# Performance work log

Measured on AMD Instinct MI355X. Metric: run time of the kernel, lower is better.

The kernel has to match this reference:

```python
import jax, jax.numpy as jnp
import numpy as np

NUM_NODES = 100000
NUM_EDGES = 1600000
IN_DIM = 128
HID = 128
OUT_DIM = 5


def setup_inputs() -> dict:
    key = jax.random.key(0)
    ks = jax.random.split(key, 8)
    x = jax.random.normal(ks[0], (NUM_NODES, IN_DIM), dtype=jnp.float32)
    edges = jax.random.randint(ks[1], (2, NUM_EDGES), 0, NUM_NODES, dtype=jnp.int32)
    s = 1.0 / np.sqrt(IN_DIM)
    W1 = jax.random.uniform(ks[2], (IN_DIM, HID), jnp.float32, -s, s)
    b1 = jax.random.uniform(ks[3], (HID,), jnp.float32, -s, s)
    sh = 1.0 / np.sqrt(HID)
    W2 = jax.random.uniform(ks[4], (HID, HID), jnp.float32, -sh, sh)
    b2 = jax.random.uniform(ks[5], (HID,), jnp.float32, -sh, sh)
    Wp = jax.random.uniform(ks[6], (HID, OUT_DIM), jnp.float32, -sh, sh)
    bp = jax.random.uniform(ks[7], (OUT_DIM,), jnp.float32, -sh, sh)
    return {"x": x, "edges": edges, "W1": W1, "b1": b1, "W2": W2, "b2": b2, "Wp": Wp, "bp": bp}


def _gnn_layer(x, src, tgt, W, b):
    # scatter-add of source features into targets (mean aggregation)
    agg = jax.ops.segment_sum(x[src], tgt, num_segments=NUM_NODES)  # [N, d]
    cnt = jax.ops.segment_sum(jnp.ones_like(tgt, dtype=x.dtype), tgt, num_segments=NUM_NODES)
    cnt = jnp.maximum(cnt, 1.0)  # clamp(min=1)
    agg = agg / cnt[:, None]
    combined = x + agg  # residual
    return jax.nn.relu(combined @ W + b)


def reference(x, edges, W1, b1, W2, b2, Wp, bp):
    src, tgt = edges[0], edges[1]
    h = _gnn_layer(x, src, tgt, W1, b1)
    h = _gnn_layer(h, src, tgt, W2, b2)
    return h @ Wp + bp  # [N, OUT_DIM]
```

## Files before the change

### kernel.cpp

```cpp
#include <hip/hip_runtime.h>

typedef unsigned int uint32;
typedef unsigned short ushort16;

typedef __attribute__((ext_vector_type(8))) short short8;
typedef __attribute__((ext_vector_type(4))) float f32x4;


#define RSH 11
#define NRG 2048
#define CAP 49152
#define CH  8192

__device__ __forceinline__ ushort16 f2bf(float f) {
    uint32 u = __float_as_uint(f);
    u += 0x7fffu + ((u >> 16) & 1u);
    return (ushort16)(u >> 16);
}
__device__ __forceinline__ float bfhi(uint32 u) { return __uint_as_float(u & 0xffff0000u); }
__device__ __forceinline__ float bflo(uint32 u) { return __uint_as_float(u << 16); }
__device__ __forceinline__ uint32 pack2(float a, float b) {
    return (uint32)f2bf(a) | ((uint32)f2bf(b) << 16);
}

union U16 { uint4 u; short8 s; };
__device__ __forceinline__ short8 ld_frag(const ushort16* p) {
    U16 x; x.u = *(const uint4*)p; return x.s;
}

#define ACC8(v) \
    acc[0] += bflo(v.x); acc[1] += bfhi(v.x); \
    acc[2] += bflo(v.y); acc[3] += bfhi(v.y); \
    acc[4] += bflo(v.z); acc[5] += bfhi(v.z); \
    acc[6] += bflo(v.w); acc[7] += bfhi(v.w);

__global__ __launch_bounds__(256)
void partition_kernel(const int* __restrict__ src, const int* __restrict__ tgt,
                      uint2* __restrict__ rlist, int* __restrict__ rcursor,
                      const float* __restrict__ W1, const float* __restrict__ W2,
                      ushort16* __restrict__ Wt1, ushort16* __restrict__ Wt2,
                      int E, int PB, int R) {
    int tid = threadIdx.x, blk = blockIdx.x;
    if (blk >= PB) {
        const float* W = (blk - PB) ? W2 : W1;
        ushort16* Wt = (blk - PB) ? Wt2 : Wt1;
        for (int i = tid; i < 16384; i += 256) {
            int k = i >> 7, c = i & 127;
            Wt[c * 128 + k] = f2bf(W[i]);
        }
        return;
    }
    __shared__ int cnt[64];
    __shared__ int cbase[64];
    for (int r = tid; r < R; r += 256) cnt[r] = 0;
    __syncthreads();
    int e0 = blk * CH, e1 = min(e0 + CH, E);
    for (int e = e0 + tid; e < e1; e += 256)
        atomicAdd(&cnt[tgt[e] >> RSH], 1);
    __syncthreads();
    for (int r = tid; r < R; r += 256) {
        cbase[r] = atomicAdd(&rcursor[r], cnt[r]);
        cnt[r] = 0;
    }
    __syncthreads();
    for (int e = e0 + tid; e < e1; e += 256) {
        int t = tgt[e];
        int r = t >> RSH;
        int sl = cbase[r] + atomicAdd(&cnt[r], 1);
        if (sl < CAP) rlist[(size_t)r * CAP + sl] = make_uint2((uint32)src[e], (uint32)t);
    }
}

template<int INF32>
__device__ __forceinline__
void gemm_body(const void* __restrict__ Asrc, const ushort16* __restrict__ Wt,
               int M, ushort16* __restrict__ outB, int bid) {
    const int tid = threadIdx.x;
    const int lane = tid & 63;
    const int wave = tid >> 6;
    const int l15 = lane & 15;
    const int quad = lane >> 4;
    const int r0 = bid * 64 + wave * 16;

    int arow = r0 + l15;
    if (arow >= M) arow = M - 1;

    short8 afr[4];
    if (INF32) {
        const float* ap = (const float*)Asrc + (size_t)arow * 128 + quad * 8;
#pragma unroll
        for (int kt = 0; kt < 4; ++kt) {
            float4 a0 = *(const float4*)(ap + kt * 32);
            float4 a1 = *(const float4*)(ap + kt * 32 + 4);
            short8 f;
            f[0] = (short)f2bf(a0.x); f[1] = (short)f2bf(a0.y);
            f[2] = (short)f2bf(a0.z); f[3] = (short)f2bf(a0.w);
            f[4] = (short)f2bf(a1.x); f[5] = (short)f2bf(a1.y);
            f[6] = (short)f2bf(a1.z); f[7] = (short)f2bf(a1.w);
            afr[kt] = f;
        }
    } else {
        const ushort16* aptr = (const ushort16*)Asrc + (size_t)arow * 128 + quad * 8;
#pragma unroll
        for (int kt = 0; kt < 4; ++kt) afr[kt] = ld_frag(aptr + kt * 32);
    }

    f32x4 acc[8];
#pragma unroll
    for (int t = 0; t < 8; ++t) acc[t] = (f32x4){0.f, 0.f, 0.f, 0.f};

#pragma unroll
    for (int t = 0; t < 8; ++t) {
        const ushort16* bptr = Wt + (size_t)(16 * t + l15) * 128 + quad * 8;
        short8 b0 = ld_frag(bptr);
        short8 b1 = ld_frag(bptr + 32);
        short8 b2 = ld_frag(bptr + 64);
        short8 b3 = ld_frag(bptr + 96);
        acc[t] = __builtin_amdgcn_mfma_f32_16x16x32_bf16(afr[0], b0, acc[t], 0, 0, 0);
        acc[t] = __builtin_amdgcn_mfma_f32_16x16x32_bf16(afr[1], b1, acc[t], 0, 0, 0);
        acc[t] = __builtin_amdgcn_mfma_f32_16x16x32_bf16(afr[2], b2, acc[t], 0, 0, 0);
        acc[t] = __builtin_amdgcn_mfma_f32_16x16x32_bf16(afr[3], b3, acc[t], 0, 0, 0);
    }

#pragma unroll
    for (int t = 0; t < 8; ++t) {
        float ov[4];
        ov[0] = acc[t].x; ov[1] = acc[t].y; ov[2] = acc[t].z; ov[3] = acc[t].w;
#pragma unroll
        for (int r = 0; r < 4; ++r) {
            float nb = __shfl_xor(ov[r], 1, 64);
            int row = r0 + quad * 4 + r;
            if (((l15 & 1) == 0) && row < M) {
                *(uint32*)(outB + (size_t)row * 128 + 16 * t + l15) = pack2(ov[r], nb);
            }
        }
    }
}

__global__ __launch_bounds__(256)
void csr_gemm1_kernel(const uint2* __restrict__ rlist, const int* __restrict__ rcursor,
                      int* __restrict__ start, int* __restrict__ deg,
                      int* __restrict__ csr, int N, int R,
                      const float* __restrict__ x, const ushort16* __restrict__ Wt1,
                      ushort16* __restrict__ ybuf) {
    int blk = blockIdx.x;
    if (blk >= R) {
        gemm_body<1>(x, Wt1, N, ybuf, blk - R);
        return;
    }
    int tid = threadIdx.x;
    __shared__ int hist[NRG];
    __shared__ int sd[256];
    __shared__ int carrySh;
    __shared__ int rbaseSh, countSh;

    int r = blk;
    if (tid == 0) {
        int rb = 0;
        for (int i = 0; i < r; ++i) rb += rcursor[i];
        rbaseSh = rb;
        countSh = min(rcursor[r], CAP);
    }
    for (int i = tid; i < NRG; i += 256) hist[i] = 0;
    __syncthreads();
    int count = countSh;
    int rbase = rbaseSh;
    const uint2* rl = rlist + (size_t)r * CAP;
    int n0 = r << RSH;

    for (int i = tid; i < count; i += 256)
        atomicAdd(&hist[rl[i].y & (NRG - 1)], 1);
    __syncthreads();

    if (tid == 0) carrySh = rbase;
    __syncthreads();
    for (int c = 0; c < 8; ++c) {
        int idx = c * 256 + tid;
        int v = hist[idx];
        int c0 = carrySh;
        sd[tid] = v;
        __syncthreads();
        for (int o = 1; o < 256; o <<= 1) {
            int t = (tid >= o) ? sd[tid - o] : 0;
            __syncthreads();
            sd[tid] += t;
            __syncthreads();
        }
        int excl = sd[tid] - v + c0;
        int tot = sd[255];
        int node = n0 + idx;
        if (node < N) { start[node] = excl; deg[node] = v; }
        hist[idx] = excl;
        __syncthreads();
        if (tid == 0) carrySh = c0 + tot;
        __syncthreads();
    }

    for (int i = tid; i < count; i += 256) {
        uint2 e = rl[i];
        int p = atomicAdd(&hist[e.y & (NRG - 1)], 1);
        csr[p] = (int)e.x;
    }
}

template<int INF32>
__global__ __launch_bounds__(256)
void gemm_raw_kernel(const void* __restrict__ Asrc, const ushort16* __restrict__ Wt,
                     int M, ushort16* __restrict__ outB) {
    gemm_body<INF32>(Asrc, Wt, M, outB, blockIdx.x);
}

template<int PROJ>
__global__ __launch_bounds__(256, 4)
void agg_fuse_kernel(const ushort16* __restrict__ hb,
                     const int* __restrict__ start, const int* __restrict__ degv,
                     const int* __restrict__ csr,
                     const float* __restrict__ bias,
                     uint32* __restrict__ outb,
                     const float* __restrict__ Wp, const float* __restrict__ bp,
                     float* __restrict__ outP, int N) {
    int wid = (blockIdx.x * 256 + threadIdx.x) >> 6;
    int lane = threadIdx.x & 63;
    if (wid >= N) return;
    int g = lane >> 4, sl = lane & 15;
    int s0 = start[wid];
    int deg = degv[wid];
    int fi = sl * 4 + g;
    uint32 su = ((const uint32*)hb)[(size_t)wid * 64 + fi];

    float acc[8];
#pragma unroll
    for (int j = 0; j < 8; ++j) acc[j] = 0.f;

    int base = 0;
    for (; base + 8 <= deg; base += 8) {
        int i0 = csr[s0 + base + g];
        int i1 = csr[s0 + base + 4 + g];
        uint4 v0 = *(const uint4*)(hb + (size_t)i0 * 128 + sl * 8);
        uint4 v1 = *(const uint4*)(hb + (size_t)i1 * 128 + sl * 8);
        ACC8(v0); ACC8(v1);
    }
    for (; base < deg; base += 4) {
        int e = base + g;
        if (e < deg) {
            int s = csr[s0 + e];
            uint4 v = *(const uint4*)(hb + (size_t)s * 128 + sl * 8);
            ACC8(v);
        }
    }
#pragma unroll
    for (int j = 0; j < 8; ++j) {
        acc[j] += __shfl_xor(acc[j], 16, 64);
        acc[j] += __shfl_xor(acc[j], 32, 64);
    }
    float inv = 1.f / fmaxf((float)deg, 1.f);
    float ax = (g == 0) ? acc[0] : (g == 1) ? acc[2] : (g == 2) ? acc[4] : acc[6];
    float ay = (g == 0) ? acc[1] : (g == 1) ? acc[3] : (g == 2) ? acc[5] : acc[7];

    float ha = fmaxf(bflo(su) + ax * inv + bias[2 * fi],     0.f);
    float hc = fmaxf(bfhi(su) + ay * inv + bias[2 * fi + 1], 0.f);

    if (!PROJ) {
        outb[(size_t)wid * 64 + fi] = pack2(ha, hc);
    } else {
        float p[5];
#pragma unroll
        for (int j = 0; j < 5; ++j)
            p[j] = ha * Wp[(2 * fi) * 5 + j] + hc * Wp[(2 * fi + 1) * 5 + j];
#pragma unroll
        for (int m = 1; m <= 32; m <<= 1)
#pragma unroll
            for (int j = 0; j < 5; ++j) p[j] += __shfl_xor(p[j], m, 64);
        if (lane == 0) {
#pragma unroll
            for (int j = 0; j < 5; ++j) outP[(size_t)wid * 5 + j] = p[j] + bp[j];
        }
    }
}

extern "C" void kernel_launch(void* const* d_in, const int* in_sizes, int n_in,
                              void* d_out, int out_size, void* d_ws, size_t ws_size,
                              hipStream_t stream) {
    const float* x     = (const float*)d_in[0];
    const int*   edges = (const int*)d_in[1];
    const float* W1    = (const float*)d_in[2];
    const float* b1    = (const float*)d_in[3];
    const float* W2    = (const float*)d_in[4];
    const float* b2    = (const float*)d_in[5];
    const float* Wp    = (const float*)d_in[6];
    const float* bp    = (const float*)d_in[7];
    float* out = (float*)d_out;

    int N = in_sizes[0] / 128;
    int E = in_sizes[1] / 2;
    const int* src = edges;
    const int* tgt = edges + E;

    const int R  = (N + NRG - 1) >> RSH;
    const int PB = (E + CH - 1) / CH;

    char* ws = (char*)d_ws;
    size_t off = 0;
    auto alloc = [&](size_t bytes) {
        char* p = ws + off;
        off = (off + bytes + 255) & ~(size_t)255;
        return p;
    };
    int*      deg     = (int*)alloc((size_t)N * 4);
    int*      start   = (int*)alloc((size_t)N * 4);
    int*      csr     = (int*)alloc((size_t)E * 4);
    uint2*    rlist   = (uint2*)alloc((size_t)R * CAP * 8);
    int*      rcursor = (int*)alloc(64 * 4);
    ushort16* ybuf    = (ushort16*)alloc((size_t)N * 128 * 2);
    ushort16* h1      = (ushort16*)alloc((size_t)N * 128 * 2);
    ushort16* Wt1     = (ushort16*)alloc(128 * 128 * 2);
    ushort16* Wt2     = (ushort16*)alloc(128 * 128 * 2);
    (void)ws_size;

    const int gemmBlocks = (N + 63) / 64;
    const int aggBlocks  = (N + 3) / 4;

    hipMemsetAsync(rcursor, 0, 64 * 4, stream);
    partition_kernel<<<PB + 2, 256, 0, stream>>>(src, tgt, rlist, rcursor,
                                                 W1, W2, Wt1, Wt2, E, PB, R);
    csr_gemm1_kernel<<<R + gemmBlocks, 256, 0, stream>>>(rlist, rcursor, start, deg,
                                                         csr, N, R, x, Wt1, ybuf);
    agg_fuse_kernel<0><<<aggBlocks, 256, 0, stream>>>(ybuf, start, deg, csr, b1,
                                                      (uint32*)h1, nullptr, nullptr,
                                                      nullptr, N);
    gemm_raw_kernel<0><<<gemmBlocks, 256, 0, stream>>>(h1, Wt2, N, ybuf);
    agg_fuse_kernel<1><<<aggBlocks, 256, 0, stream>>>(ybuf, start, deg, csr, b2,
                                                      nullptr, Wp, bp, out, N);
}
```

Baseline: 387.3 us.

## Split edge partition into count, scan, scatter passes and widen CSR build blocks

Replaces the single partition kernel, which used global atomic cursors, with three passes: per-chunk bucket counts, a per-bucket scan across chunks, and a deterministic scatter that reads int4-vectorized edges. Chunk size shrinks to raise parallelism, and the weight transpose is spread over 16 blocks. The CSR build kernel now uses 1024-thread blocks with a 4-way unrolled histogram/scatter and a wave-shuffle prefix for the bucket base. This adds two kernel launches and an extra pass over tgt in exchange for more parallel, contention-free partitioning. Vector loads assume E divisible by 4.

Measured after the change: 325.3 us. -16.0%, faster.

```diff
diff --git a/kernel.cpp b/kernel.cpp
--- a/kernel.cpp
+++ b/kernel.cpp
@@ -10,7 +10,7 @@
 #define RSH 11
 #define NRG 2048
 #define CAP 49152
-#define CH  8192
+#define CH  2048
 
 __device__ __forceinline__ ushort16 f2bf(float f) {
     uint32 u = __float_as_uint(f);
@@ -35,54 +35,111 @@
     acc[6] += bflo(v.w); acc[7] += bfhi(v.w);
 
 __global__ __launch_bounds__(256)
-void partition_kernel(const int* __restrict__ src, const int* __restrict__ tgt,
-                      uint2* __restrict__ rlist, int* __restrict__ rcursor,
-                      const float* __restrict__ W1, const float* __restrict__ W2,
-                      ushort16* __restrict__ Wt1, ushort16* __restrict__ Wt2,
-                      int E, int PB, int R) {
+void count_prep_kernel(const int* __restrict__ tgt, int* __restrict__ hist,
+                       const float* __restrict__ W1, const float* __restrict__ W2,
+                       ushort16* __restrict__ Wt1, ushort16* __restrict__ Wt2,
+                       int E, int PB, int R) {
     int tid = threadIdx.x, blk = blockIdx.x;
     if (blk >= PB) {
-        const float* W = (blk - PB) ? W2 : W1;
-        ushort16* Wt = (blk - PB) ? Wt2 : Wt1;
-        for (int i = tid; i < 16384; i += 256) {
-            int k = i >> 7, c = i & 127;
-            Wt[c * 128 + k] = f2bf(W[i]);
-        }
+        int idx = blk - PB;
+        const float* W = (idx >> 3) ? W2 : W1;
+        ushort16* Wt = (idx >> 3) ? Wt2 : Wt1;
+        int i0 = (idx & 7) * 2048 + tid * 8;
+        float4 a = *(const float4*)(W + i0);
+        float4 b = *(const float4*)(W + i0 + 4);
+        int k = i0 >> 7, col = i0 & 127;
+        Wt[(col + 0) * 128 + k] = f2bf(a.x);
+        Wt[(col + 1) * 128 + k] = f2bf(a.y);
+        Wt[(col + 2) * 128 + k] = f2bf(a.z);
+        Wt[(col + 3) * 128 + k] = f2bf(a.w);
+        Wt[(col + 4) * 128 + k] = f2bf(b.x);
+        Wt[(col + 5) * 128 + k] = f2bf(b.y);
+        Wt[(col + 6) * 128 + k] = f2bf(b.z);
+        Wt[(col + 7) * 128 + k] = f2bf(b.w);
         return;
     }
     __shared__ int cnt[64];
-    __shared__ int cbase[64];
-    for (int r = tid; r < R; r += 256) cnt[r] = 0;
-    __syncthreads();
-    int e0 = blk * CH, e1 = min(e0 + CH, E);
-    for (int e = e0 + tid; e < e1; e += 256)
-        atomicAdd(&cnt[tgt[e] >> RSH], 1);
-    __syncthreads();
-    for (int r = tid; r < R; r += 256) {
-        cbase[r] = atomicAdd(&rcursor[r], cnt[r]);
-        cnt[r] = 0;
-    }
-    __syncthreads();
-    for (int e = e0 + tid; e < e1; e += 256) {
-        int t = tgt[e];
-        int r = t >> RSH;
-        int sl = cbase[r] + atomicAdd(&cnt[r], 1);
-        if (sl < CAP) rlist[(size_t)r * CAP + sl] = make_uint2((uint32)src[e], (uint32)t);
+    if (tid < 64) cnt[tid] = 0;
+    __syncthreads();
+    int q0 = blk * (CH / 4), q1 = min(q0 + CH / 4, E / 4);
+    for (int q = q0 + tid; q < q1; q += 256) {
+        int4 t = ((const int4*)tgt)[q];
+        atomicAdd(&cnt[t.x >> RSH], 1);
+        atomicAdd(&cnt[t.y >> RSH], 1);
+        atomicAdd(&cnt[t.z >> RSH], 1);
+        atomicAdd(&cnt[t.w >> RSH], 1);
+    }
+    __syncthreads();
+    if (tid < R) hist[(size_t)blk * 64 + tid] = cnt[tid];
+}
+
+__global__ __launch_bounds__(256)
+void scan_kernel(int* __restrict__ hist, int* __restrict__ total, int PB) {
+    __shared__ int sd[256];
+    __shared__ int carrySh;
+    int r = blockIdx.x, tid = threadIdx.x;
+    if (tid == 0) carrySh = 0;
+    __syncthreads();
+    int chunks = (PB + 255) >> 8;
+    for (int ch = 0; ch < chunks; ++ch) {
+        int g = ch * 256 + tid;
+        int v = (g < PB) ? hist[(size_t)g * 64 + r] : 0;
+        int c0 = carrySh;
+        sd[tid] = v;
+        __syncthreads();
+        for (int o = 1; o < 256; o <<= 1) {
+            int t = (tid >= o) ? sd[tid - o] : 0;
+            __syncthreads();
+            sd[tid] += t;
+            __syncthreads();
+        }
+        if (g < PB) hist[(size_t)g * 64 + r] = sd[tid] - v + c0;
+        int tot = sd[255];
+        __syncthreads();
+        if (tid == 0) carrySh = c0 + tot;
+        __syncthreads();
+    }
+    if (tid == 0) total[r] = carrySh;
+}
+
+__global__ __launch_bounds__(256)
+void scatter_kernel(const int* __restrict__ src, const int* __restrict__ tgt,
+                    const int* __restrict__ hist, uint2* __restrict__ rlist,
+                    int E, int R) {
+    __shared__ int cb[64];
+    __shared__ int cnt[64];
+    int tid = threadIdx.x, blk = blockIdx.x;
+    if (tid < 64) {
+        cnt[tid] = 0;
+        cb[tid] = (tid < R) ? hist[(size_t)blk * 64 + tid] : 0;
+    }
+    __syncthreads();
+    int q0 = blk * (CH / 4), q1 = min(q0 + CH / 4, E / 4);
+    for (int q = q0 + tid; q < q1; q += 256) {
+        int4 t = ((const int4*)tgt)[q];
+        int4 s = ((const int4*)src)[q];
+        int r0 = t.x >> RSH, r1 = t.y >> RSH, r2 = t.z >> RSH, r3 = t.w >> RSH;
+        int l0 = atomicAdd(&cnt[r0], 1);
+        int l1 = atomicAdd(&cnt[r1], 1);
+        int l2 = atomicAdd(&cnt[r2], 1);
+        int l3 = atomicAdd(&cnt[r3], 1);
+        int p0 = cb[r0] + l0, p1 = cb[r1] + l1, p2 = cb[r2] + l2, p3 = cb[r3] + l3;
+        if (p0 < CAP) rlist[(size_t)r0 * CAP + p0] = make_uint2((uint32)s.x, (uint32)t.x);
+        if (p1 < CAP) rlist[(size_t)r1 * CAP + p1] = make_uint2((uint32)s.y, (uint32)t.y);
+        if (p2 < CAP) rlist[(size_t)r2 * CAP + p2] = make_uint2((uint32)s.z, (uint32)t.z);
+        if (p3 < CAP) rlist[(size_t)r3 * CAP + p3] = make_uint2((uint32)s.w, (uint32)t.w);
     }
 }
 
 template<int INF32>
 __device__ __forceinline__
-void gemm_body(const void* __restrict__ Asrc, const ushort16* __restrict__ Wt,
-               int M, ushort16* __restrict__ outB, int bid) {
-    const int tid = threadIdx.x;
-    const int lane = tid & 63;
-    const int wave = tid >> 6;
+void gemm_rows(const void* __restrict__ Asrc, const ushort16* __restrict__ Wt,
+               int M, ushort16* __restrict__ outB, int r0w) {
+    const int lane = threadIdx.x & 63;
     const int l15 = lane & 15;
     const int quad = lane >> 4;
-    const int r0 = bid * 64 + wave * 16;
-
-    int arow = r0 + l15;
+
+    int arow = r0w + l15;
     if (arow >= M) arow = M - 1;
 
     short8 afr[4];
@@ -129,7 +186,7 @@
 #pragma unroll
         for (int r = 0; r < 4; ++r) {
             float nb = __shfl_xor(ov[r], 1, 64);
-            int row = r0 + quad * 4 + r;
+            int row = r0w + quad * 4 + r;
             if (((l15 & 1) == 0) && row < M) {
                 *(uint32*)(outB + (size_t)row * 128 + 16 * t + l15) = pack2(ov[r], nb);
             }
@@ -137,69 +194,95 @@
     }
 }
 
-__global__ __launch_bounds__(256)
-void csr_gemm1_kernel(const uint2* __restrict__ rlist, const int* __restrict__ rcursor,
+__global__ __launch_bounds__(1024)
+void csr_gemm1_kernel(const uint2* __restrict__ rlist, const int* __restrict__ total,
                       int* __restrict__ start, int* __restrict__ deg,
                       int* __restrict__ csr, int N, int R,
                       const float* __restrict__ x, const ushort16* __restrict__ Wt1,
                       ushort16* __restrict__ ybuf) {
     int blk = blockIdx.x;
+    int tid = threadIdx.x;
     if (blk >= R) {
-        gemm_body<1>(x, Wt1, N, ybuf, blk - R);
+        int gid = blk - R;
+        gemm_rows<1>(x, Wt1, N, ybuf, gid * 256 + (tid >> 6) * 16);
         return;
     }
-    int tid = threadIdx.x;
     __shared__ int hist[NRG];
-    __shared__ int sd[256];
+    __shared__ int sd[1024];
     __shared__ int carrySh;
     __shared__ int rbaseSh, countSh;
 
     int r = blk;
-    if (tid == 0) {
-        int rb = 0;
-        for (int i = 0; i < r; ++i) rb += rcursor[i];
-        rbaseSh = rb;
-        countSh = min(rcursor[r], CAP);
-    }
-    for (int i = tid; i < NRG; i += 256) hist[i] = 0;
+    if (tid == 0) countSh = min(total[r], CAP);
+    if (tid < 64) {
+        int v = (tid < R) ? total[tid] : 0;
+        int pm = (tid < r) ? v : 0;
+#pragma unroll
+        for (int o = 1; o < 64; o <<= 1) pm += __shfl_xor(pm, o, 64);
+        if (tid == 0) rbaseSh = pm;
+    }
+    for (int i = tid; i < NRG; i += 1024) hist[i] = 0;
     __syncthreads();
     int count = countSh;
-    int rbase = rbaseSh;
     const uint2* rl = rlist + (size_t)r * CAP;
     int n0 = r << RSH;
 
-    for (int i = tid; i < count; i += 256)
-        atomicAdd(&hist[rl[i].y & (NRG - 1)], 1);
-    __syncthreads();
-
-    if (tid == 0) carrySh = rbase;
-    __syncthreads();
-    for (int c = 0; c < 8; ++c) {
-        int idx = c * 256 + tid;
+    {
+        int i = tid;
+        for (; i + 3072 < count; i += 4096) {
+            uint2 a = rl[i], b = rl[i + 1024], c = rl[i + 2048], d = rl[i + 3072];
+            atomicAdd(&hist[a.y & (NRG - 1)], 1);
+            atomicAdd(&hist[b.y & (NRG - 1)], 1);
+            atomicAdd(&hist[c.y & (NRG - 1)], 1);
+            atomicAdd(&hist[d.y & (NRG - 1)], 1);
+        }
+        for (; i < count; i += 1024)
+            atomicAdd(&hist[rl[i].y & (NRG - 1)], 1);
+    }
+    __syncthreads();
+
+    if (tid == 0) carrySh = rbaseSh;
+    __syncthreads();
+    for (int ch = 0; ch < 2; ++ch) {
+        int idx = ch * 1024 + tid;
         int v = hist[idx];
         int c0 = carrySh;
         sd[tid] = v;
         __syncthreads();
-        for (int o = 1; o < 256; o <<= 1) {
+        for (int o = 1; o < 1024; o <<= 1) {
             int t = (tid >= o) ? sd[tid - o] : 0;
             __syncthreads();
             sd[tid] += t;
             __syncthreads();
         }
         int excl = sd[tid] - v + c0;
-        int tot = sd[255];
+        int tot = sd[1023];
         int node = n0 + idx;
         if (node < N) { start[node] = excl; deg[node] = v; }
+        __syncthreads();
         hist[idx] = excl;
-        __syncthreads();
         if (tid == 0) carrySh = c0 + tot;
         __syncthreads();
     }
 
-    for (int i = tid; i < count; i += 256) {
-        uint2 e = rl[i];
-        int p = atomicAdd(&hist[e.y & (NRG - 1)], 1);
-        csr[p] = (int)e.x;
+    {
+        int i = tid;
+        for (; i + 3072 < count; i += 4096) {
+            uint2 a = rl[i], b = rl[i + 1024], c = rl[i + 2048], d = rl[i + 3072];
+            int pa = atomicAdd(&hist[a.y & (NRG - 1)], 1);
+            int pb = atomicAdd(&hist[b.y & (NRG - 1)], 1);
+            int pc = atomicAdd(&hist[c.y & (NRG - 1)], 1);
+            int pd = atomicAdd(&hist[d.y & (NRG - 1)], 1);
+            csr[pa] = (int)a.x;
+            csr[pb] = (int)b.x;
+            csr[pc] = (int)c.x;
+            csr[pd] = (int)d.x;
+        }
+        for (; i < count; i += 1024) {
+            uint2 e = rl[i];
+            int p = atomicAdd(&hist[e.y & (NRG - 1)], 1);
+            csr[p] = (int)e.x;
+        }
     }
 }
 
@@ -207,7 +290,7 @@
 __global__ __launch_bounds__(256)
 void gemm_raw_kernel(const void* __restrict__ Asrc, const ushort16* __restrict__ Wt,
                      int M, ushort16* __restrict__ outB) {
-    gemm_body<INF32>(Asrc, Wt, M, outB, blockIdx.x);
+    gemm_rows<INF32>(Asrc, Wt, M, outB, blockIdx.x * 64 + (threadIdx.x >> 6) * 16);
 }
 
 template<int PROJ>
@@ -310,21 +393,24 @@
     int*      start   = (int*)alloc((size_t)N * 4);
     int*      csr     = (int*)alloc((size_t)E * 4);
     uint2*    rlist   = (uint2*)alloc((size_t)R * CAP * 8);
-    int*      rcursor = (int*)alloc(64 * 4);
+    int*      hist    = (int*)alloc((size_t)PB * 64 * 4);
+    int*      total   = (int*)alloc(64 * 4);
     ushort16* ybuf    = (ushort16*)alloc((size_t)N * 128 * 2);
     ushort16* h1      = (ushort16*)alloc((size_t)N * 128 * 2);
     ushort16* Wt1     = (ushort16*)alloc(128 * 128 * 2);
     ushort16* Wt2     = (ushort16*)alloc(128 * 128 * 2);
     (void)ws_size;
 
+    const int g1Blocks   = (N + 255) / 256;
     const int gemmBlocks = (N + 63) / 64;
     const int aggBlocks  = (N + 3) / 4;
 
-    hipMemsetAsync(rcursor, 0, 64 * 4, stream);
-    partition_kernel<<<PB + 2, 256, 0, stream>>>(src, tgt, rlist, rcursor,
-                                                 W1, W2, Wt1, Wt2, E, PB, R);
-    csr_gemm1_kernel<<<R + gemmBlocks, 256, 0, stream>>>(rlist, rcursor, start, deg,
-                                                         csr, N, R, x, Wt1, ybuf);
+    count_prep_kernel<<<PB + 16, 256, 0, stream>>>(tgt, hist, W1, W2, Wt1, Wt2,
+                                                   E, PB, R);
+    scan_kernel<<<R, 256, 0, stream>>>(hist, total, PB);
+    scatter_kernel<<<PB, 256, 0, stream>>>(src, tgt, hist, rlist, E, R);
+    csr_gemm1_kernel<<<R + g1Blocks, 1024, 0, stream>>>(rlist, total, start, deg,
+                                                        csr, N, R, x, Wt1, ybuf);
     agg_fuse_kernel<0><<<aggBlocks, 256, 0, stream>>>(ybuf, start, deg, csr, b1,
                                                       (uint32*)h1, nullptr, nullptr,
                                                       nullptr, N);
```
